# Kernel tuning notes

Measured on AMD Instinct MI355X. Metric: run time of the kernel, lower is better.

Reference implementation:

```python
import jax, jax.numpy as jnp
import numpy as np

B, T, V, H, L = 4, 2048, 32000, 512, 2

def setup_inputs() -> dict:
    key = jax.random.key(0)
    ks = jax.random.split(key, 8)
    s = 0.04  # ~1/sqrt(H) scaling to keep tanh unsaturated
    return {
        "x": jax.random.randint(ks[0], (B, T), 0, V, dtype=jnp.int32),
        "embed": jax.random.normal(ks[1], (V, H), jnp.float32) * s,
        "W_ih": jax.random.normal(ks[2], (L, H, H), jnp.float32) * s,
        "b_ih": jax.random.normal(ks[3], (L, H), jnp.float32) * s,
        "W_hh": jax.random.normal(ks[4], (L, H, H), jnp.float32) * s,
        "b_hh": jax.random.normal(ks[5], (L, H), jnp.float32) * s,
        "W_out": jax.random.normal(ks[6], (V, H), jnp.float32) * s,
        "b_out": jax.random.normal(ks[7], (V,), jnp.float32) * s,
    }

def reference(x, embed, W_ih, b_ih, W_hh, b_hh, W_out, b_out):
    emb = embed[x]                      # [B, T, H]
    num_layers = W_ih.shape[0]
    Bsz = x.shape[0]
    Hd = embed.shape[1]

    def step(h, x_t):                   # h: [L, B, H], x_t: [B, H]
        inp = x_t
        new_h = []
        for l in range(num_layers):     # small fixed layer count
            hl = jnp.tanh(inp @ W_ih[l].T + b_ih[l] + h[l] @ W_hh[l].T + b_hh[l])
            new_h.append(hl)
            inp = hl
        out = inp @ W_out.T + b_out     # [B, V]
        return jnp.stack(new_h), out

    h0 = jnp.zeros((num_layers, Bsz, Hd), emb.dtype)
    h_final, outs = jax.lax.scan(step, h0, jnp.swapaxes(emb, 0, 1))  # outs: [T, B, V]
    return jnp.swapaxes(outs, 0, 1), h_final
```

## Files before the change

kernel.cpp:

```cpp
#include <hip/hip_runtime.h>
#include <stdint.h>

#define Bdim 4
#define Tdim 2048
#define Vdim 32000
#define Hdim 512
#define MROWS (Bdim * Tdim)

typedef unsigned short u16;
typedef __bf16 bf16x8 __attribute__((ext_vector_type(8)));
typedef float f32x4 __attribute__((ext_vector_type(4)));

__device__ __forceinline__ u16 f2bf(float f) {
  union { float f; uint32_t u; } a; a.f = f;
  uint32_t r = a.u + 0x7FFFu + ((a.u >> 16) & 1u);
  return (u16)(r >> 16);
}
__device__ __forceinline__ float bf2f(uint32_t lo16) {
  union { uint32_t u; float f; } a; a.u = lo16 << 16;
  return a.f;
}

__global__ void k_gather(const int* __restrict__ x, const float* __restrict__ embed,
                         u16* __restrict__ E) {
  int idx = blockIdx.x * 256 + threadIdx.x;
  int row = idx >> 7;
  int c4  = (idx & 127) << 2;
  int tok = x[row];
  const float4 v = *(const float4*)(embed + (size_t)tok * Hdim + c4);
  *(ushort4*)(E + (size_t)row * Hdim + c4) =
      make_ushort4(f2bf(v.x), f2bf(v.y), f2bf(v.z), f2bf(v.w));
}

__global__ void k_f2b(const float* __restrict__ in, u16* __restrict__ out, int n4) {
  int idx = blockIdx.x * 256 + threadIdx.x;
  if (idx >= n4) return;
  const float4 v = *(const float4*)(in + (size_t)idx * 4);
  *(ushort4*)(out + (size_t)idx * 4) =
      make_ushort4(f2bf(v.x), f2bf(v.y), f2bf(v.z), f2bf(v.w));
}

__device__ __forceinline__ void g2l16(const void* g, void* l) {
  __builtin_amdgcn_global_load_lds(
      (const __attribute__((address_space(1))) uint32_t*)g,
      (__attribute__((address_space(3))) uint32_t*)l, 16, 0, 0);
}

__global__ __launch_bounds__(256, 2) void k_gemm(
    const u16* __restrict__ A, const u16* __restrict__ Bw, float* __restrict__ C,
    const float* __restrict__ bias1, const float* __restrict__ bias2,
    int M, int N, int K, int ntN)
{
  __shared__ u16 Al[128 * 64];
  __shared__ u16 Bl[128 * 64];
  const int bid = blockIdx.x;
  const int mt = bid / ntN, nt = bid % ntN;
  const int m0 = mt << 7, n0 = nt << 7;
  const int tid = threadIdx.x;
  const int l = tid & 63, w = tid >> 6;
  const int wy = w >> 1, wx = w & 1;
  const int frow = l & 15, fk = (l >> 4) << 3;

  f32x4 acc[4][4];
  #pragma unroll
  for (int a = 0; a < 4; ++a)
    #pragma unroll
    for (int b = 0; b < 4; ++b) acc[a][b] = f32x4{0.f, 0.f, 0.f, 0.f};

  for (int kb = 0; kb < K; kb += 64) {
    __syncthreads();
    #pragma unroll
    for (int is = 0; is < 4; ++is) {
      const int off = tid * 16 + is * 4096;
      const int lrow = off >> 7, lcolB = off & 127;
      g2l16(A  + (size_t)(m0 + lrow) * K + kb + (lcolB >> 1), (char*)Al + off);
      g2l16(Bw + (size_t)(n0 + lrow) * K + kb + (lcolB >> 1), (char*)Bl + off);
    }
    __syncthreads();
    #pragma unroll
    for (int ks = 0; ks < 2; ++ks) {
      bf16x8 af[4], bfr[4];
      #pragma unroll
      for (int mi = 0; mi < 4; ++mi)
        af[mi] = *(const bf16x8*)&Al[((wy * 64 + mi * 16 + frow) << 6) + ks * 32 + fk];
      #pragma unroll
      for (int ni = 0; ni < 4; ++ni)
        bfr[ni] = *(const bf16x8*)&Bl[((wx * 64 + ni * 16 + frow) << 6) + ks * 32 + fk];
      #pragma unroll
      for (int mi = 0; mi < 4; ++mi)
        #pragma unroll
        for (int ni = 0; ni < 4; ++ni)
          acc[mi][ni] = __builtin_amdgcn_mfma_f32_16x16x32_bf16(af[mi], bfr[ni], acc[mi][ni], 0, 0, 0);
    }
  }
  #pragma unroll
  for (int ni = 0; ni < 4; ++ni) {
    const int col = n0 + wx * 64 + ni * 16 + (l & 15);
    float bv = bias1[col];
    if (bias2) bv += bias2[col];
    #pragma unroll
    for (int mi = 0; mi < 4; ++mi) {
      const int row = m0 + wy * 64 + mi * 16 + ((l >> 4) << 2);
      #pragma unroll
      for (int r = 0; r < 4; ++r)
        C[(size_t)(row + r) * N + col] = acc[mi][ni][r] + bv;
    }
  }
}

#define SENT 0xFFFFFFFFu

__device__ __forceinline__ uint32_t aload(const uint32_t* p) {
  return __hip_atomic_load(p, __ATOMIC_RELAXED, __HIP_MEMORY_SCOPE_AGENT);
}
__device__ __forceinline__ void astore(uint32_t* p, uint32_t v) {
  __hip_atomic_store(p, v, __ATOMIC_RELAXED, __HIP_MEMORY_SCOPE_AGENT);
}

template <bool L1>
__device__ void scan_layer(const float* __restrict__ X0,
                           const float* __restrict__ WA,
                           const float* __restrict__ WB,
                           const float* __restrict__ bi1, const float* __restrict__ bi2,
                           uint32_t* __restrict__ H0b, uint32_t* __restrict__ H1b,
                           float* __restrict__ hfin, int slice)
{
  constexpr int KCH = L1 ? 32 : 16;
  constexpr int SEG = KCH * 4;
  __shared__ float hs[Bdim * 1024];
  const int tid = threadIdx.x;
  const int b  = tid >> 7;
  const int r  = tid & 127;
  const int i  = r >> 3;
  const int kq = r & 7;
  const int ig = slice * 16 + i;

  float wv[SEG];
  #pragma unroll
  for (int c = 0; c < KCH; ++c) {
    const int cc = (c + kq) & (KCH - 1);
    #pragma unroll
    for (int e = 0; e < 4; ++e) {
      const int k = kq * SEG + cc * 4 + e;
      if constexpr (L1) {
        wv[c * 4 + e] = (k < Hdim) ? WA[(size_t)ig * Hdim + k]
                                   : WB[(size_t)ig * Hdim + (k - Hdim)];
      } else {
        wv[c * 4 + e] = WA[(size_t)ig * Hdim + k];
      }
    }
  }
  float extra_c = 0.f;
  if constexpr (L1) extra_c = bi1[ig] + bi2[ig];

  #pragma unroll
  for (int j = 0; j < (Bdim * 1024) / 512; ++j) hs[tid + j * 512] = 0.f;
  __syncthreads();

  uint32_t* const Hout = L1 ? H1b : H0b;
  const int w0 = tid, w1 = tid + 512;
  const int b0 = w0 >> 8, q0 = w0 & 255;
  const int b1 = w1 >> 8, q1 = w1 & 255;

  for (int t = 0; t < Tdim; ++t) {
    float extra = extra_c;
    if constexpr (!L1) extra = X0[(size_t)(b * Tdim + t) * Hdim + ig];

    if constexpr (L1) {
      const uint32_t* p0 = &H0b[(size_t)(b0 * Tdim + t) * 256 + q0];
      const uint32_t* p1 = &H0b[(size_t)(b1 * Tdim + t) * 256 + q1];
      uint32_t v0 = aload(p0), v1 = aload(p1), v2 = 0, v3 = 0;
      const uint32_t *p2 = p0, *p3 = p1;
      if (t > 0) {
        p2 = &H1b[(size_t)(b0 * Tdim + (t - 1)) * 256 + q0];
        p3 = &H1b[(size_t)(b1 * Tdim + (t - 1)) * 256 + q1];
        v2 = aload(p2); v3 = aload(p3);
      }
      while (v0 == SENT) v0 = aload(p0);
      while (v1 == SENT) v1 = aload(p1);
      if (t > 0) {
        while (v2 == SENT) v2 = aload(p2);
        while (v3 == SENT) v3 = aload(p3);
      }
      __syncthreads();
      *(float2*)&hs[b0 * 1024 + q0 * 2] = make_float2(bf2f(v0 & 0xFFFF), bf2f(v0 >> 16));
      *(float2*)&hs[b1 * 1024 + q1 * 2] = make_float2(bf2f(v1 & 0xFFFF), bf2f(v1 >> 16));
      if (t > 0) {
        *(float2*)&hs[b0 * 1024 + 512 + q0 * 2] = make_float2(bf2f(v2 & 0xFFFF), bf2f(v2 >> 16));
        *(float2*)&hs[b1 * 1024 + 512 + q1 * 2] = make_float2(bf2f(v3 & 0xFFFF), bf2f(v3 >> 16));
      }
      __syncthreads();
    } else {
      if (t > 0) {
        const uint32_t* p0 = &H0b[(size_t)(b0 * Tdim + (t - 1)) * 256 + q0];
        const uint32_t* p1 = &H0b[(size_t)(b1 * Tdim + (t - 1)) * 256 + q1];
        uint32_t v0 = aload(p0), v1 = aload(p1);
        while (v0 == SENT) v0 = aload(p0);
        while (v1 == SENT) v1 = aload(p1);
        __syncthreads();
        *(float2*)&hs[b0 * 1024 + q0 * 2] = make_float2(bf2f(v0 & 0xFFFF), bf2f(v0 >> 16));
        *(float2*)&hs[b1 * 1024 + q1 * 2] = make_float2(bf2f(v1 & 0xFFFF), bf2f(v1 >> 16));
        __syncthreads();
      }
    }

    float sum = 0.f;
    const float* hb = hs + b * 1024;
    #pragma unroll
    for (int c = 0; c < KCH; ++c) {
      const int cc = (c + kq) & (KCH - 1);
      const float4 hv = *(const float4*)&hb[kq * SEG + cc * 4];
      sum = fmaf(wv[c * 4 + 0], hv.x, sum);
      sum = fmaf(wv[c * 4 + 1], hv.y, sum);
      sum = fmaf(wv[c * 4 + 2], hv.z, sum);
      sum = fmaf(wv[c * 4 + 3], hv.w, sum);
    }
    sum += __shfl_xor(sum, 1);
    sum += __shfl_xor(sum, 2);
    sum += __shfl_xor(sum, 4);
    const float h  = tanhf(sum + extra);
    const float hp = __shfl_down(h, 8);
    if (kq == 0) {
      if ((i & 1) == 0) {
        const uint32_t wd = (uint32_t)f2bf(h) | ((uint32_t)f2bf(hp) << 16);
        astore(&Hout[(size_t)(b * Tdim + t) * 256 + (ig >> 1)], wd);
      }
      if (t == Tdim - 1)
        hfin[(L1 ? 1 : 0) * (Bdim * Hdim) + b * Hdim + ig] = h;
    }
  }
}

__global__ __launch_bounds__(512, 2) void k_scan(
    const float* __restrict__ X0, const float* __restrict__ W_ih,
    const float* __restrict__ W_hh, const float* __restrict__ b_ih,
    const float* __restrict__ b_hh, uint32_t* __restrict__ H0b,
    uint32_t* __restrict__ H1b, float* __restrict__ hfin)
{
  const int blk = blockIdx.x;
  if (blk < 32) {
    scan_layer<false>(X0, W_hh, nullptr, nullptr, nullptr, H0b, H1b, hfin, blk);
  } else {
    scan_layer<true>(nullptr, W_ih + Hdim * Hdim, W_hh + Hdim * Hdim,
                     b_ih + Hdim, b_hh + Hdim, H0b, H1b, hfin, blk - 32);
  }
}

extern "C" void kernel_launch(void* const* d_in, const int* in_sizes, int n_in,
                              void* d_out, int out_size, void* d_ws, size_t ws_size,
                              hipStream_t stream)
{
  const int*   x     = (const int*)d_in[0];
  const float* embed = (const float*)d_in[1];
  const float* W_ih  = (const float*)d_in[2];
  const float* b_ih  = (const float*)d_in[3];
  const float* W_hh  = (const float*)d_in[4];
  const float* b_hh  = (const float*)d_in[5];
  const float* W_out = (const float*)d_in[6];
  const float* b_out = (const float*)d_in[7];
  float* out = (float*)d_out;

  char* ws = (char*)d_ws;
  u16* E       = (u16*)ws;
  u16* Wih0b   = E + (size_t)MROWS * Hdim;
  u16* Woutb   = Wih0b + Hdim * Hdim;
  float* X0    = (float*)(Woutb + (size_t)Vdim * Hdim);
  uint32_t* H0b = (uint32_t*)(X0 + (size_t)MROWS * Hdim);
  uint32_t* H1b = H0b + (size_t)MROWS * (Hdim / 2);

  k_gather<<<MROWS * (Hdim / 4) / 256, 256, 0, stream>>>(x, embed, E);
  k_f2b<<<(Hdim * Hdim / 4) / 256, 256, 0, stream>>>(W_ih, Wih0b, Hdim * Hdim / 4);
  k_f2b<<<(Vdim * Hdim / 4) / 256, 256, 0, stream>>>(W_out, Woutb, Vdim * Hdim / 4);

  k_gemm<<<(MROWS / 128) * (Hdim / 128), 256, 0, stream>>>(
      E, Wih0b, X0, b_ih, b_hh, MROWS, Hdim, Hdim, Hdim / 128);

  hipMemsetAsync(H0b, 0xFF, (size_t)MROWS * (Hdim / 2) * 4, stream);
  hipMemsetAsync(H1b, 0xFF, (size_t)MROWS * (Hdim / 2) * 4, stream);

  float* hfin = out + (size_t)MROWS * Vdim;
  k_scan<<<64, 512, 0, stream>>>(X0, W_ih, W_hh, b_ih, b_hh, H0b, H1b, hfin);

  k_gemm<<<(MROWS / 128) * (Vdim / 128), 256, 0, stream>>>(
      (const u16*)H1b, Woutb, out, b_out, nullptr, MROWS, Vdim, Hdim, Vdim / 128);
}
```

Measured before the change: 5.938 ms.

## Rewrite recurrent scan as single-wave MFMA blocks with bf16 register-resident weights

```diff
diff --git a/kernel.cpp b/kernel.cpp
--- a/kernel.cpp
+++ b/kernel.cpp
@@ -15,10 +15,6 @@
   union { float f; uint32_t u; } a; a.f = f;
   uint32_t r = a.u + 0x7FFFu + ((a.u >> 16) & 1u);
   return (u16)(r >> 16);
-}
-__device__ __forceinline__ float bf2f(uint32_t lo16) {
-  union { uint32_t u; float f; } a; a.u = lo16 << 16;
-  return a.f;
 }
 
 __global__ void k_gather(const int* __restrict__ x, const float* __restrict__ embed,
@@ -117,133 +113,153 @@
   __hip_atomic_store(p, v, __ATOMIC_RELAXED, __HIP_MEMORY_SCOPE_AGENT);
 }
 
-template <bool L1>
-__device__ void scan_layer(const float* __restrict__ X0,
-                           const float* __restrict__ WA,
-                           const float* __restrict__ WB,
-                           const float* __restrict__ bi1, const float* __restrict__ bi2,
-                           uint32_t* __restrict__ H0b, uint32_t* __restrict__ H1b,
-                           float* __restrict__ hfin, int slice)
+template <bool IS_L1>
+__device__ __forceinline__ void scan_wave(
+    const float* __restrict__ X0,
+    const float* __restrict__ W1,
+    const float* __restrict__ W2,
+    const float* __restrict__ bi1, const float* __restrict__ bi2,
+    uint32_t* __restrict__ H0b, uint32_t* __restrict__ H1b,
+    float* __restrict__ hfin, int slice, u16* hs)
 {
-  constexpr int KCH = L1 ? 32 : 16;
-  constexpr int SEG = KCH * 4;
-  __shared__ float hs[Bdim * 1024];
-  const int tid = threadIdx.x;
-  const int b  = tid >> 7;
-  const int r  = tid & 127;
-  const int i  = r >> 3;
-  const int kq = r & 7;
-  const int ig = slice * 16 + i;
-
-  float wv[SEG];
+  constexpr int NB   = IS_L1 ? 32 : 16;
+  constexpr int SROW = IS_L1 ? 1040 : 528;
+  const int l  = threadIdx.x;
+  const int n  = l & 15;
+  const int cq = l >> 4;
+  const int ng = slice * 16 + n;
+  const int fb = n & 3;
+  const int pb = cq, pw = n;
+
+  bf16x8 bw[NB];
   #pragma unroll
-  for (int c = 0; c < KCH; ++c) {
-    const int cc = (c + kq) & (KCH - 1);
-    #pragma unroll
-    for (int e = 0; e < 4; ++e) {
-      const int k = kq * SEG + cc * 4 + e;
-      if constexpr (L1) {
-        wv[c * 4 + e] = (k < Hdim) ? WA[(size_t)ig * Hdim + k]
-                                   : WB[(size_t)ig * Hdim + (k - Hdim)];
-      } else {
-        wv[c * 4 + e] = WA[(size_t)ig * Hdim + k];
-      }
-    }
+  for (int j = 0; j < NB; ++j) {
+    const float* wrow;
+    int koff;
+    if constexpr (IS_L1) {
+      if (j < 16) { wrow = W1 + (size_t)ng * Hdim; koff = j * 32; }
+      else        { wrow = W2 + (size_t)ng * Hdim; koff = (j - 16) * 32; }
+    } else        { wrow = W1 + (size_t)ng * Hdim; koff = j * 32; }
+    const float4 a = *(const float4*)(wrow + koff + cq * 8);
+    const float4 b = *(const float4*)(wrow + koff + cq * 8 + 4);
+    bw[j][0] = (__bf16)a.x; bw[j][1] = (__bf16)a.y;
+    bw[j][2] = (__bf16)a.z; bw[j][3] = (__bf16)a.w;
+    bw[j][4] = (__bf16)b.x; bw[j][5] = (__bf16)b.y;
+    bw[j][6] = (__bf16)b.z; bw[j][7] = (__bf16)b.w;
   }
-  float extra_c = 0.f;
-  if constexpr (L1) extra_c = bi1[ig] + bi2[ig];
-
-  #pragma unroll
-  for (int j = 0; j < (Bdim * 1024) / 512; ++j) hs[tid + j * 512] = 0.f;
-  __syncthreads();
-
-  uint32_t* const Hout = L1 ? H1b : H0b;
-  const int w0 = tid, w1 = tid + 512;
-  const int b0 = w0 >> 8, q0 = w0 & 255;
-  const int b1 = w1 >> 8, q1 = w1 & 255;
+  float bias = 0.f;
+  if constexpr (IS_L1) bias = bi1[ng] + bi2[ng];
+
+  uint32_t* const Hout = IS_L1 ? H1b : H0b;
 
   for (int t = 0; t < Tdim; ++t) {
-    float extra = extra_c;
-    if constexpr (!L1) extra = X0[(size_t)(b * Tdim + t) * Hdim + ig];
-
-    if constexpr (L1) {
-      const uint32_t* p0 = &H0b[(size_t)(b0 * Tdim + t) * 256 + q0];
-      const uint32_t* p1 = &H0b[(size_t)(b1 * Tdim + t) * 256 + q1];
-      uint32_t v0 = aload(p0), v1 = aload(p1), v2 = 0, v3 = 0;
-      const uint32_t *p2 = p0, *p3 = p1;
+    float x0v[4];
+    if constexpr (!IS_L1) {
+      #pragma unroll
+      for (int b = 0; b < 4; ++b)
+        x0v[b] = X0[((size_t)b * Tdim + t) * Hdim + ng];
+    }
+    f32x4 ac[4];
+    #pragma unroll
+    for (int q = 0; q < 4; ++q) ac[q] = f32x4{0.f, 0.f, 0.f, 0.f};
+
+    if constexpr (!IS_L1) {
       if (t > 0) {
-        p2 = &H1b[(size_t)(b0 * Tdim + (t - 1)) * 256 + q0];
-        p3 = &H1b[(size_t)(b1 * Tdim + (t - 1)) * 256 + q1];
-        v2 = aload(p2); v3 = aload(p3);
-      }
-      while (v0 == SENT) v0 = aload(p0);
-      while (v1 == SENT) v1 = aload(p1);
+        const uint32_t* P = H0b + ((size_t)pb * Tdim + (t - 1)) * 256 + pw;
+        uint32_t v[16];
+        #pragma unroll
+        for (int m = 0; m < 16; ++m) v[m] = aload(P + m * 16);
+        #pragma unroll
+        for (int m = 0; m < 16; ++m) while (v[m] == SENT) v[m] = aload(P + m * 16);
+        __syncthreads();
+        #pragma unroll
+        for (int m = 0; m < 16; ++m)
+          *(uint32_t*)&hs[pb * SROW + 2 * (pw + m * 16)] = v[m];
+        __syncthreads();
+        #pragma unroll
+        for (int j = 0; j < 16; ++j) {
+          const bf16x8 af = *(const bf16x8*)&hs[fb * SROW + j * 32 + cq * 8];
+          ac[j & 3] = __builtin_amdgcn_mfma_f32_16x16x32_bf16(af, bw[j], ac[j & 3], 0, 0, 0);
+        }
+      }
+    } else {
+      const uint32_t* P0 = H0b + ((size_t)pb * Tdim + t) * 256 + pw;
+      const uint32_t* P1 = H1b + ((size_t)pb * Tdim + (t - 1)) * 256 + pw;
+      uint32_t v[16], u[16];
+      #pragma unroll
+      for (int m = 0; m < 16; ++m) v[m] = aload(P0 + m * 16);
       if (t > 0) {
-        while (v2 == SENT) v2 = aload(p2);
-        while (v3 == SENT) v3 = aload(p3);
-      }
+        #pragma unroll
+        for (int m = 0; m < 16; ++m) u[m] = aload(P1 + m * 16);
+      }
+      #pragma unroll
+      for (int m = 0; m < 16; ++m) while (v[m] == SENT) v[m] = aload(P0 + m * 16);
       __syncthreads();
-      *(float2*)&hs[b0 * 1024 + q0 * 2] = make_float2(bf2f(v0 & 0xFFFF), bf2f(v0 >> 16));
-      *(float2*)&hs[b1 * 1024 + q1 * 2] = make_float2(bf2f(v1 & 0xFFFF), bf2f(v1 >> 16));
+      #pragma unroll
+      for (int m = 0; m < 16; ++m)
+        *(uint32_t*)&hs[pb * SROW + 2 * (pw + m * 16)] = v[m];
+      __syncthreads();
+      #pragma unroll
+      for (int j = 0; j < 16; ++j) {
+        const bf16x8 af = *(const bf16x8*)&hs[fb * SROW + j * 32 + cq * 8];
+        ac[j & 3] = __builtin_amdgcn_mfma_f32_16x16x32_bf16(af, bw[j], ac[j & 3], 0, 0, 0);
+      }
       if (t > 0) {
-        *(float2*)&hs[b0 * 1024 + 512 + q0 * 2] = make_float2(bf2f(v2 & 0xFFFF), bf2f(v2 >> 16));
-        *(float2*)&hs[b1 * 1024 + 512 + q1 * 2] = make_float2(bf2f(v3 & 0xFFFF), bf2f(v3 >> 16));
-      }
-      __syncthreads();
-    } else {
-      if (t > 0) {
-        const uint32_t* p0 = &H0b[(size_t)(b0 * Tdim + (t - 1)) * 256 + q0];
-        const uint32_t* p1 = &H0b[(size_t)(b1 * Tdim + (t - 1)) * 256 + q1];
-        uint32_t v0 = aload(p0), v1 = aload(p1);
-        while (v0 == SENT) v0 = aload(p0);
-        while (v1 == SENT) v1 = aload(p1);
+        #pragma unroll
+        for (int m = 0; m < 16; ++m) while (u[m] == SENT) u[m] = aload(P1 + m * 16);
         __syncthreads();
-        *(float2*)&hs[b0 * 1024 + q0 * 2] = make_float2(bf2f(v0 & 0xFFFF), bf2f(v0 >> 16));
-        *(float2*)&hs[b1 * 1024 + q1 * 2] = make_float2(bf2f(v1 & 0xFFFF), bf2f(v1 >> 16));
+        #pragma unroll
+        for (int m = 0; m < 16; ++m)
+          *(uint32_t*)&hs[pb * SROW + 512 + 2 * (pw + m * 16)] = u[m];
         __syncthreads();
-      }
-    }
-
-    float sum = 0.f;
-    const float* hb = hs + b * 1024;
-    #pragma unroll
-    for (int c = 0; c < KCH; ++c) {
-      const int cc = (c + kq) & (KCH - 1);
-      const float4 hv = *(const float4*)&hb[kq * SEG + cc * 4];
-      sum = fmaf(wv[c * 4 + 0], hv.x, sum);
-      sum = fmaf(wv[c * 4 + 1], hv.y, sum);
-      sum = fmaf(wv[c * 4 + 2], hv.z, sum);
-      sum = fmaf(wv[c * 4 + 3], hv.w, sum);
-    }
-    sum += __shfl_xor(sum, 1);
-    sum += __shfl_xor(sum, 2);
-    sum += __shfl_xor(sum, 4);
-    const float h  = tanhf(sum + extra);
-    const float hp = __shfl_down(h, 8);
-    if (kq == 0) {
-      if ((i & 1) == 0) {
-        const uint32_t wd = (uint32_t)f2bf(h) | ((uint32_t)f2bf(hp) << 16);
-        astore(&Hout[(size_t)(b * Tdim + t) * 256 + (ig >> 1)], wd);
-      }
-      if (t == Tdim - 1)
-        hfin[(L1 ? 1 : 0) * (Bdim * Hdim) + b * Hdim + ig] = h;
+        #pragma unroll
+        for (int j = 16; j < 32; ++j) {
+          const bf16x8 af = *(const bf16x8*)&hs[fb * SROW + j * 32 + cq * 8];
+          ac[j & 3] = __builtin_amdgcn_mfma_f32_16x16x32_bf16(af, bw[j], ac[j & 3], 0, 0, 0);
+        }
+      }
+    }
+
+    const f32x4 acc = (ac[0] + ac[1]) + (ac[2] + ac[3]);
+    float hv[4], hp[4];
+    #pragma unroll
+    for (int r = 0; r < 4; ++r) {
+      float ex;
+      if constexpr (IS_L1) ex = bias; else ex = x0v[r];
+      hv[r] = tanhf(acc[r] + ex);
+    }
+    #pragma unroll
+    for (int r = 0; r < 4; ++r) hp[r] = __shfl_xor(hv[r], 1);
+    if (cq == 0) {
+      if (!(n & 1)) {
+        #pragma unroll
+        for (int r = 0; r < 4; ++r) {
+          const uint32_t wd = (uint32_t)f2bf(hv[r]) | ((uint32_t)f2bf(hp[r]) << 16);
+          astore(&Hout[((size_t)r * Tdim + t) * 256 + (ng >> 1)], wd);
+        }
+      }
+      if (t == Tdim - 1) {
+        #pragma unroll
+        for (int r = 0; r < 4; ++r)
+          hfin[(IS_L1 ? Bdim * Hdim : 0) + r * Hdim + ng] = hv[r];
+      }
     }
   }
 }
 
-__global__ __launch_bounds__(512, 2) void k_scan(
+__global__ __launch_bounds__(64, 1) void k_scan(
     const float* __restrict__ X0, const float* __restrict__ W_ih,
     const float* __restrict__ W_hh, const float* __restrict__ b_ih,
     const float* __restrict__ b_hh, uint32_t* __restrict__ H0b,
     uint32_t* __restrict__ H1b, float* __restrict__ hfin)
 {
+  __shared__ u16 hs[4160];
   const int blk = blockIdx.x;
-  if (blk < 32) {
-    scan_layer<false>(X0, W_hh, nullptr, nullptr, nullptr, H0b, H1b, hfin, blk);
-  } else {
-    scan_layer<true>(nullptr, W_ih + Hdim * Hdim, W_hh + Hdim * Hdim,
-                     b_ih + Hdim, b_hh + Hdim, H0b, H1b, hfin, blk - 32);
-  }
+  if (blk < 32)
+    scan_wave<false>(X0, W_hh, nullptr, nullptr, nullptr, H0b, H1b, hfin, blk, hs);
+  else
+    scan_wave<true>(nullptr, W_ih + Hdim * Hdim, W_hh + Hdim * Hdim,
+                    b_ih + Hdim, b_hh + Hdim, H0b, H1b, hfin, blk - 32, hs);
 }
 
 extern "C" void kernel_launch(void* const* d_in, const int* in_sizes, int n_in,
@@ -279,7 +295,7 @@
   hipMemsetAsync(H1b, 0xFF, (size_t)MROWS * (Hdim / 2) * 4, stream);
 
   float* hfin = out + (size_t)MROWS * Vdim;
-  k_scan<<<64, 512, 0, stream>>>(X0, W_ih, W_hh, b_ih, b_hh, H0b, H1b, hfin);
+  k_scan<<<64, 64, 0, stream>>>(X0, W_ih, W_hh, b_ih, b_hh, H0b, H1b, hfin);
 
   k_gemm<<<(MROWS / 128) * (Vdim / 128), 256, 0, stream>>>(
       (const u16*)H1b, Woutb, out, b_out, nullptr, MROWS, Vdim, Hdim, Vdim / 128);
```

Result: slower. 9.842 ms (+65.7%).

## Rewrite recurrent scan as single-wave MFMA with time-major hidden buffers

Applied to the files above, without the earlier changes.

```diff
diff --git a/kernel.cpp b/kernel.cpp
--- a/kernel.cpp
+++ b/kernel.cpp
@@ -15,10 +15,6 @@
   union { float f; uint32_t u; } a; a.f = f;
   uint32_t r = a.u + 0x7FFFu + ((a.u >> 16) & 1u);
   return (u16)(r >> 16);
-}
-__device__ __forceinline__ float bf2f(uint32_t lo16) {
-  union { uint32_t u; float f; } a; a.u = lo16 << 16;
-  return a.f;
 }
 
 __global__ void k_gather(const int* __restrict__ x, const float* __restrict__ embed,
@@ -49,7 +45,7 @@
 __global__ __launch_bounds__(256, 2) void k_gemm(
     const u16* __restrict__ A, const u16* __restrict__ Bw, float* __restrict__ C,
     const float* __restrict__ bias1, const float* __restrict__ bias2,
-    int M, int N, int K, int ntN)
+    int M, int N, int K, int ntN, int aperm)
 {
   __shared__ u16 Al[128 * 64];
   __shared__ u16 Bl[128 * 64];
@@ -73,7 +69,11 @@
     for (int is = 0; is < 4; ++is) {
       const int off = tid * 16 + is * 4096;
       const int lrow = off >> 7, lcolB = off & 127;
-      g2l16(A  + (size_t)(m0 + lrow) * K + kb + (lcolB >> 1), (char*)Al + off);
+      const int mrow = m0 + lrow;
+      const size_t arow = aperm
+          ? (size_t)(mrow & 2047) * 2048 + (size_t)(mrow >> 11) * 512
+          : (size_t)mrow * K;
+      g2l16(A  + arow + kb + (lcolB >> 1), (char*)Al + off);
       g2l16(Bw + (size_t)(n0 + lrow) * K + kb + (lcolB >> 1), (char*)Bl + off);
     }
     __syncthreads();
@@ -110,140 +110,146 @@
 
 #define SENT 0xFFFFFFFFu
 
-__device__ __forceinline__ uint32_t aload(const uint32_t* p) {
+__device__ __forceinline__ uint64_t al64(const uint64_t* p) {
   return __hip_atomic_load(p, __ATOMIC_RELAXED, __HIP_MEMORY_SCOPE_AGENT);
 }
 __device__ __forceinline__ void astore(uint32_t* p, uint32_t v) {
   __hip_atomic_store(p, v, __ATOMIC_RELAXED, __HIP_MEMORY_SCOPE_AGENT);
 }
-
-template <bool L1>
-__device__ void scan_layer(const float* __restrict__ X0,
-                           const float* __restrict__ WA,
-                           const float* __restrict__ WB,
-                           const float* __restrict__ bi1, const float* __restrict__ bi2,
-                           uint32_t* __restrict__ H0b, uint32_t* __restrict__ H1b,
-                           float* __restrict__ hfin, int slice)
-{
-  constexpr int KCH = L1 ? 32 : 16;
-  constexpr int SEG = KCH * 4;
-  __shared__ float hs[Bdim * 1024];
-  const int tid = threadIdx.x;
-  const int b  = tid >> 7;
-  const int r  = tid & 127;
-  const int i  = r >> 3;
-  const int kq = r & 7;
-  const int ig = slice * 16 + i;
-
-  float wv[SEG];
-  #pragma unroll
-  for (int c = 0; c < KCH; ++c) {
-    const int cc = (c + kq) & (KCH - 1);
-    #pragma unroll
-    for (int e = 0; e < 4; ++e) {
-      const int k = kq * SEG + cc * 4 + e;
-      if constexpr (L1) {
-        wv[c * 4 + e] = (k < Hdim) ? WA[(size_t)ig * Hdim + k]
-                                   : WB[(size_t)ig * Hdim + (k - Hdim)];
-      } else {
-        wv[c * 4 + e] = WA[(size_t)ig * Hdim + k];
-      }
-    }
-  }
-  float extra_c = 0.f;
-  if constexpr (L1) extra_c = bi1[ig] + bi2[ig];
-
-  #pragma unroll
-  for (int j = 0; j < (Bdim * 1024) / 512; ++j) hs[tid + j * 512] = 0.f;
-  __syncthreads();
-
-  uint32_t* const Hout = L1 ? H1b : H0b;
-  const int w0 = tid, w1 = tid + 512;
-  const int b0 = w0 >> 8, q0 = w0 & 255;
-  const int b1 = w1 >> 8, q1 = w1 & 255;
-
+__device__ __forceinline__ bool fbad(uint64_t a, uint64_t b) {
+  return ((uint32_t)a == SENT) | ((uint32_t)(a >> 32) == SENT) |
+         ((uint32_t)b == SENT) | ((uint32_t)(b >> 32) == SENT);
+}
+__device__ __forceinline__ bf16x8 fuse2(uint64_t a, uint64_t b) {
+  union { uint64_t u[2]; bf16x8 h; } U;
+  U.u[0] = a; U.u[1] = b;
+  return U.h;
+}
+__device__ __forceinline__ float fast_tanh(float x) {
+  float e = __expf(2.f * x);
+  return 1.f - 2.f * __builtin_amdgcn_rcpf(e + 1.f);
+}
+
+#define FISSUE(base64, va, vb)                                   \
+  _Pragma("unroll")                                              \
+  for (int j = 0; j < 16; ++j) {                                 \
+    const uint64_t* _p = (base64) + j * 8 + cq * 2;              \
+    va[j] = al64(_p); vb[j] = al64(_p + 1);                      \
+  }
+#define FCONSUME(base64, va, vb, W)                              \
+  _Pragma("unroll")                                              \
+  for (int j = 0; j < 16; ++j) {                                 \
+    const uint64_t* _p = (base64) + j * 8 + cq * 2;              \
+    while (fbad(va[j], vb[j])) { va[j] = al64(_p); vb[j] = al64(_p + 1); } \
+    ac[j & 3] = __builtin_amdgcn_mfma_f32_16x16x32_bf16(                   \
+        fuse2(va[j], vb[j]), W[j], ac[j & 3], 0, 0, 0);                    \
+  }
+
+__device__ __forceinline__ float sel4(f32x4 s, int cq) {
+  float r = s[0];
+  r = cq == 1 ? s[1] : r;
+  r = cq == 2 ? s[2] : r;
+  r = cq == 3 ? s[3] : r;
+  return r;
+}
+
+__device__ void scan_l0(const float* __restrict__ X0, const u16* __restrict__ Whh0,
+                        uint32_t* __restrict__ H0b, float* __restrict__ hfin,
+                        int slice) {
+  const int l = threadIdx.x, n = l & 15, cq = l >> 4;
+  const int ng = slice * 16 + n, fb = n & 3;
+  bf16x8 bw[16];
+  #pragma unroll
+  for (int j = 0; j < 16; ++j)
+    bw[j] = *(const bf16x8*)&Whh0[(size_t)ng * Hdim + j * 32 + cq * 8];
+  uint64_t va[16], vb[16];
+  float x0v = X0[((size_t)cq * Tdim) * Hdim + ng];
+
+  #pragma unroll 1
   for (int t = 0; t < Tdim; ++t) {
-    float extra = extra_c;
-    if constexpr (!L1) extra = X0[(size_t)(b * Tdim + t) * Hdim + ig];
-
-    if constexpr (L1) {
-      const uint32_t* p0 = &H0b[(size_t)(b0 * Tdim + t) * 256 + q0];
-      const uint32_t* p1 = &H0b[(size_t)(b1 * Tdim + t) * 256 + q1];
-      uint32_t v0 = aload(p0), v1 = aload(p1), v2 = 0, v3 = 0;
-      const uint32_t *p2 = p0, *p3 = p1;
-      if (t > 0) {
-        p2 = &H1b[(size_t)(b0 * Tdim + (t - 1)) * 256 + q0];
-        p3 = &H1b[(size_t)(b1 * Tdim + (t - 1)) * 256 + q1];
-        v2 = aload(p2); v3 = aload(p3);
-      }
-      while (v0 == SENT) v0 = aload(p0);
-      while (v1 == SENT) v1 = aload(p1);
-      if (t > 0) {
-        while (v2 == SENT) v2 = aload(p2);
-        while (v3 == SENT) v3 = aload(p3);
-      }
-      __syncthreads();
-      *(float2*)&hs[b0 * 1024 + q0 * 2] = make_float2(bf2f(v0 & 0xFFFF), bf2f(v0 >> 16));
-      *(float2*)&hs[b1 * 1024 + q1 * 2] = make_float2(bf2f(v1 & 0xFFFF), bf2f(v1 >> 16));
-      if (t > 0) {
-        *(float2*)&hs[b0 * 1024 + 512 + q0 * 2] = make_float2(bf2f(v2 & 0xFFFF), bf2f(v2 >> 16));
-        *(float2*)&hs[b1 * 1024 + 512 + q1 * 2] = make_float2(bf2f(v3 & 0xFFFF), bf2f(v3 >> 16));
-      }
-      __syncthreads();
-    } else {
-      if (t > 0) {
-        const uint32_t* p0 = &H0b[(size_t)(b0 * Tdim + (t - 1)) * 256 + q0];
-        const uint32_t* p1 = &H0b[(size_t)(b1 * Tdim + (t - 1)) * 256 + q1];
-        uint32_t v0 = aload(p0), v1 = aload(p1);
-        while (v0 == SENT) v0 = aload(p0);
-        while (v1 == SENT) v1 = aload(p1);
-        __syncthreads();
-        *(float2*)&hs[b0 * 1024 + q0 * 2] = make_float2(bf2f(v0 & 0xFFFF), bf2f(v0 >> 16));
-        *(float2*)&hs[b1 * 1024 + q1 * 2] = make_float2(bf2f(v1 & 0xFFFF), bf2f(v1 >> 16));
-        __syncthreads();
-      }
-    }
-
-    float sum = 0.f;
-    const float* hb = hs + b * 1024;
-    #pragma unroll
-    for (int c = 0; c < KCH; ++c) {
-      const int cc = (c + kq) & (KCH - 1);
-      const float4 hv = *(const float4*)&hb[kq * SEG + cc * 4];
-      sum = fmaf(wv[c * 4 + 0], hv.x, sum);
-      sum = fmaf(wv[c * 4 + 1], hv.y, sum);
-      sum = fmaf(wv[c * 4 + 2], hv.z, sum);
-      sum = fmaf(wv[c * 4 + 3], hv.w, sum);
-    }
-    sum += __shfl_xor(sum, 1);
-    sum += __shfl_xor(sum, 2);
-    sum += __shfl_xor(sum, 4);
-    const float h  = tanhf(sum + extra);
-    const float hp = __shfl_down(h, 8);
-    if (kq == 0) {
-      if ((i & 1) == 0) {
-        const uint32_t wd = (uint32_t)f2bf(h) | ((uint32_t)f2bf(hp) << 16);
-        astore(&Hout[(size_t)(b * Tdim + t) * 256 + (ig >> 1)], wd);
-      }
-      if (t == Tdim - 1)
-        hfin[(L1 ? 1 : 0) * (Bdim * Hdim) + b * Hdim + ig] = h;
-    }
-  }
-}
-
-__global__ __launch_bounds__(512, 2) void k_scan(
-    const float* __restrict__ X0, const float* __restrict__ W_ih,
-    const float* __restrict__ W_hh, const float* __restrict__ b_ih,
+    float x0n = 0.f;
+    if (t + 1 < Tdim) x0n = X0[((size_t)cq * Tdim + t + 1) * Hdim + ng];
+    f32x4 ac[4];
+    ac[0] = ac[1] = ac[2] = ac[3] = f32x4{0.f, 0.f, 0.f, 0.f};
+    if (t > 0) {
+      const uint64_t* pb = (const uint64_t*)H0b + (size_t)(t - 1) * 512 + fb * 128;
+      FCONSUME(pb, va, vb, bw);
+    }
+    const f32x4 s4 = (ac[0] + ac[1]) + (ac[2] + ac[3]);
+    const float hsel = fast_tanh(sel4(s4, cq) + x0v);
+    const float hp = __shfl_xor(hsel, 1);
+    if (!(n & 1))
+      astore(H0b + (size_t)t * 1024 + cq * 256 + (ng >> 1),
+             (uint32_t)f2bf(hsel) | ((uint32_t)f2bf(hp) << 16));
+    if (t == Tdim - 1) hfin[cq * Hdim + ng] = hsel;
+    if (t + 1 < Tdim) {
+      const uint64_t* pb = (const uint64_t*)H0b + (size_t)t * 512 + fb * 128;
+      FISSUE(pb, va, vb);
+    }
+    x0v = x0n;
+  }
+}
+
+__device__ void scan_l1(const u16* __restrict__ Wih1, const u16* __restrict__ Whh1,
+                        const float* __restrict__ bi1, const float* __restrict__ bi2,
+                        uint32_t* __restrict__ H0b, uint32_t* __restrict__ H1b,
+                        float* __restrict__ hfin, int slice) {
+  const int l = threadIdx.x, n = l & 15, cq = l >> 4;
+  const int ng = slice * 16 + n, fb = n & 3;
+  bf16x8 bw[16], ww[16];
+  #pragma unroll
+  for (int j = 0; j < 16; ++j) {
+    bw[j] = *(const bf16x8*)&Whh1[(size_t)ng * Hdim + j * 32 + cq * 8];
+    ww[j] = *(const bf16x8*)&Wih1[(size_t)ng * Hdim + j * 32 + cq * 8];
+  }
+  const float bias = bi1[ng] + bi2[ng];
+  uint64_t ua[16], ub[16];
+  uint64_t wa[16], wb[16];
+  { const uint64_t* p0 = (const uint64_t*)H0b + fb * 128; FISSUE(p0, ua, ub); }
+
+  #pragma unroll 1
+  for (int t = 0; t < Tdim; ++t) {
+    if (t > 0) {
+      const uint64_t* p1 = (const uint64_t*)H1b + (size_t)(t - 1) * 512 + fb * 128;
+      FISSUE(p1, wa, wb);
+    }
+    f32x4 ac[4];
+    ac[0] = f32x4{bias, bias, bias, bias};
+    ac[1] = ac[2] = ac[3] = f32x4{0.f, 0.f, 0.f, 0.f};
+    {
+      const uint64_t* p0 = (const uint64_t*)H0b + (size_t)t * 512 + fb * 128;
+      FCONSUME(p0, ua, ub, ww);
+    }
+    if (t + 1 < Tdim) {
+      const uint64_t* p0 = (const uint64_t*)H0b + (size_t)(t + 1) * 512 + fb * 128;
+      FISSUE(p0, ua, ub);
+    }
+    if (t > 0) {
+      const uint64_t* p1 = (const uint64_t*)H1b + (size_t)(t - 1) * 512 + fb * 128;
+      FCONSUME(p1, wa, wb, bw);
+    }
+    const f32x4 s4 = (ac[0] + ac[1]) + (ac[2] + ac[3]);
+    const float hsel = fast_tanh(sel4(s4, cq));
+    const float hp = __shfl_xor(hsel, 1);
+    if (!(n & 1))
+      astore(H1b + (size_t)t * 1024 + cq * 256 + (ng >> 1),
+             (uint32_t)f2bf(hsel) | ((uint32_t)f2bf(hp) << 16));
+    if (t == Tdim - 1) hfin[Bdim * Hdim + cq * Hdim + ng] = hsel;
+  }
+}
+
+__global__ __launch_bounds__(64) void k_scan(
+    const float* __restrict__ X0, const u16* __restrict__ Wihb,
+    const u16* __restrict__ Whhb, const float* __restrict__ b_ih,
     const float* __restrict__ b_hh, uint32_t* __restrict__ H0b,
     uint32_t* __restrict__ H1b, float* __restrict__ hfin)
 {
   const int blk = blockIdx.x;
-  if (blk < 32) {
-    scan_layer<false>(X0, W_hh, nullptr, nullptr, nullptr, H0b, H1b, hfin, blk);
-  } else {
-    scan_layer<true>(nullptr, W_ih + Hdim * Hdim, W_hh + Hdim * Hdim,
-                     b_ih + Hdim, b_hh + Hdim, H0b, H1b, hfin, blk - 32);
-  }
+  if (blk < 32)
+    scan_l0(X0, Whhb, H0b, hfin, blk);
+  else
+    scan_l1(Wihb + Hdim * Hdim, Whhb + Hdim * Hdim, b_ih + Hdim, b_hh + Hdim,
+            H0b, H1b, hfin, blk - 32);
 }
 
 extern "C" void kernel_launch(void* const* d_in, const int* in_sizes, int n_in,
@@ -262,25 +268,27 @@
 
   char* ws = (char*)d_ws;
   u16* E       = (u16*)ws;
-  u16* Wih0b   = E + (size_t)MROWS * Hdim;
-  u16* Woutb   = Wih0b + Hdim * Hdim;
+  u16* Wihb    = E + (size_t)MROWS * Hdim;
+  u16* Whhb    = Wihb + 2 * Hdim * Hdim;
+  u16* Woutb   = Whhb + 2 * Hdim * Hdim;
   float* X0    = (float*)(Woutb + (size_t)Vdim * Hdim);
   uint32_t* H0b = (uint32_t*)(X0 + (size_t)MROWS * Hdim);
-  uint32_t* H1b = H0b + (size_t)MROWS * (Hdim / 2);
+  uint32_t* H1b = H0b + (size_t)Tdim * 1024;
+
+  hipMemsetAsync(H0b, 0xFF, (size_t)Tdim * 1024 * 4, stream);
+  hipMemsetAsync(H1b, 0xFF, (size_t)Tdim * 1024 * 4, stream);
 
   k_gather<<<MROWS * (Hdim / 4) / 256, 256, 0, stream>>>(x, embed, E);
-  k_f2b<<<(Hdim * Hdim / 4) / 256, 256, 0, stream>>>(W_ih, Wih0b, Hdim * Hdim / 4);
-  k_f2b<<<(Vdim * Hdim / 4) / 256, 256, 0, stream>>>(W_out, Woutb, Vdim * Hdim / 4);
+  k_f2b<<<(2 * Hdim * Hdim / 4) / 256, 256, 0, stream>>>(W_ih, Wihb, 2 * Hdim * Hdim / 4);
+  k_f2b<<<(2 * Hdim * Hdim / 4) / 256, 256, 0, stream>>>(W_hh, Whhb, 2 * Hdim * Hdim / 4);
+  k_f2b<<<((size_t)Vdim * Hdim / 4) / 256, 256, 0, stream>>>(W_out, Woutb, Vdim * Hdim / 4);
 
   k_gemm<<<(MROWS / 128) * (Hdim / 128), 256, 0, stream>>>(
-      E, Wih0b, X0, b_ih, b_hh, MROWS, Hdim, Hdim, Hdim / 128);
-
-  hipMemsetAsync(H0b, 0xFF, (size_t)MROWS * (Hdim / 2) * 4, stream);
-  hipMemsetAsync(H1b, 0xFF, (size_t)MROWS * (Hdim / 2) * 4, stream);
+      E, Wihb, X0, b_ih, b_hh, MROWS, Hdim, Hdim, Hdim / 128, 0);
 
   float* hfin = out + (size_t)MROWS * Vdim;
-  k_scan<<<64, 512, 0, stream>>>(X0, W_ih, W_hh, b_ih, b_hh, H0b, H1b, hfin);
+  k_scan<<<64, 64, 0, stream>>>(X0, Wihb, Whhb, b_ih, b_hh, H0b, H1b, hfin);
 
   k_gemm<<<(MROWS / 128) * (Vdim / 128), 256, 0, stream>>>(
-      (const u16*)H1b, Woutb, out, b_out, nullptr, MROWS, Vdim, Hdim, Vdim / 128);
-}
+      (const u16*)H1b, Woutb, out, b_out, nullptr, MROWS, Vdim, Hdim, Vdim / 128, 1);
+}
```

After: 10.96 ms. 1.85x slower.
